# Performance work log

Measured on AMD Instinct MI355X. Metric: run time of the kernel, lower is better.

Reference implementation:

```python
import jax, jax.numpy as jnp
import numpy as np


def setup_inputs() -> dict:
    key = jax.random.key(0)
    k1, k2 = jax.random.split(key)
    N, D, K = 262144, 64, 1024
    residual = jax.random.normal(k1, (N, D), dtype=jnp.float32)
    # nn.init.uniform_(codebook.weight, -1/K, 1/K)
    codebook = jax.random.uniform(k2, (K, D), dtype=jnp.float32,
                                  minval=-1.0 / K, maxval=1.0 / K)
    return {"residual": residual, "codebook": codebook}


def reference(residual, codebook):
    # squared L2 distances via ||a||^2 + ||b||^2 - 2 a.b (argmin-equivalent to
    # the broadcast (N,K,D) form, without materializing it)
    r2 = jnp.sum(residual * residual, axis=1, keepdims=True)        # (N, 1)
    c2 = jnp.sum(codebook * codebook, axis=1)[None, :]              # (1, K)
    dists = r2 + c2 - 2.0 * (residual @ codebook.T)                 # (N, K)
    codes = jnp.argmin(dists, axis=1)                               # (N,) int
    quantized = codebook[codes]                                     # (N, D)
    return quantized, codes
```

## Files before the change

kernel.cpp:

```cpp
#include <hip/hip_runtime.h>
#include <float.h>

#define D 64

typedef float f32x4 __attribute__((ext_vector_type(4)));
typedef _Float16 f16x8 __attribute__((ext_vector_type(8)));

__device__ __forceinline__ float np_sum_sq_64(const float* v) {
  float s[8];
#pragma unroll
  for (int j = 0; j < 8; ++j) s[j] = __fmul_rn(v[j], v[j]);
#pragma unroll
  for (int b = 1; b < 8; ++b) {
#pragma unroll
    for (int j = 0; j < 8; ++j)
      s[j] = __fadd_rn(s[j], __fmul_rn(v[8 * b + j], v[8 * b + j]));
  }
  float t01 = __fadd_rn(s[0], s[1]);
  float t23 = __fadd_rn(s[2], s[3]);
  float t45 = __fadd_rn(s[4], s[5]);
  float t67 = __fadd_rn(s[6], s[7]);
  return __fadd_rn(__fadd_rn(t01, t23), __fadd_rn(t45, t67));
}

__device__ __forceinline__ unsigned int pkh(float a, float b) {
  union { _Float16 h[2]; unsigned int u; } x;
  x.h[0] = (_Float16)a;
  x.h[1] = (_Float16)b;
  return x.u;
}

__global__ __launch_bounds__(64) void vq_prep(
    const float* __restrict__ cb, unsigned short* __restrict__ cbh,
    float4* __restrict__ cbT4, float* __restrict__ c2,
    float* __restrict__ c2n, unsigned int* __restrict__ counters, int K) {
  if (blockIdx.x == 0 && threadIdx.x == 0) { counters[0] = 0u; counters[1] = 0u; }
  int k = blockIdx.x * 64 + threadIdx.x;
  if (k >= K) return;
  float row[D];
  const float4* cp = (const float4*)(cb + (size_t)k * D);
#pragma unroll
  for (int i = 0; i < 16; ++i) {
    float4 v = cp[i];
    row[4 * i] = v.x; row[4 * i + 1] = v.y;
    row[4 * i + 2] = v.z; row[4 * i + 3] = v.w;
    cbT4[(size_t)i * K + k] = v;
    *(uint2*)(cbh + (size_t)k * D + 4 * i) =
        make_uint2(pkh(v.x * 1024.f, v.y * 1024.f),
                   pkh(v.z * 1024.f, v.w * 1024.f));
  }
  float c2v = np_sum_sq_64(row);
  c2[k] = c2v;
  c2n[k] = -512.0f * c2v;
}

__global__ __launch_bounds__(256, 3) void vq_screen(
    const float* __restrict__ residual, const float* __restrict__ codebook,
    const unsigned short* __restrict__ cbh, const float* __restrict__ c2n,
    float* __restrict__ out_q, float* __restrict__ codes_f,
    unsigned int* __restrict__ counters, int* __restrict__ list,
    int N, int K) {
  __shared__ unsigned short smem[4096];
  __shared__ float red[768];
  __shared__ int code_lds[64];
  __shared__ float srow[64];

  int tid = threadIdx.x;
  int rowbase = blockIdx.x * 64;

  float sr4[4];
#pragma unroll
  for (int jj = 0; jj < 4; ++jj) {
    int i = tid + 256 * jj;
    int r = i >> 4, d0 = (i & 15) * 4;
    float4 v = *(const float4*)(residual + (size_t)(rowbase + r) * D + d0);
    sr4[jj] = fabsf(v.x) + fabsf(v.y) + fabsf(v.z) + fabsf(v.w);
    int tile = r >> 4, rr = r & 15;
    int kblk = d0 >> 5, kk = d0 & 31;
    int lanep = rr + 16 * (kk >> 3);
    int off = ((tile * 2 + kblk) * 64 + lanep) * 8 + (kk & 7);
    *(uint2*)(smem + off) = make_uint2(pkh(v.x, v.y), pkh(v.z, v.w));
  }
#pragma unroll
  for (int jj = 0; jj < 4; ++jj) {
    float s = sr4[jj];
    s += __shfl_xor(s, 1, 64);
    s += __shfl_xor(s, 2, 64);
    s += __shfl_xor(s, 4, 64);
    s += __shfl_xor(s, 8, 64);
    sr4[jj] = s;
  }
  if ((tid & 15) == 0) {
#pragma unroll
    for (int jj = 0; jj < 4; ++jj) srow[(tid >> 4) + 16 * jj] = sr4[jj];
  }
  __syncthreads();

  int w = tid >> 6, lane = tid & 63;
  int lane15 = lane & 15, lq = lane >> 4;

  f16x8 ah[4][2];
#pragma unroll
  for (int t = 0; t < 4; ++t)
#pragma unroll
    for (int kb = 0; kb < 2; ++kb)
      ah[t][kb] = *(const f16x8*)(smem + ((t * 2 + kb) * 64 + lane) * 8);

  float m1[4][4], m2[4][4], m3[4][4];
#pragma unroll
  for (int t = 0; t < 4; ++t)
#pragma unroll
    for (int j = 0; j < 4; ++j) {
      m1[t][j] = -FLT_MAX; m2[t][j] = -FLT_MAX; m3[t][j] = -FLT_MAX;
    }

  const unsigned short* ph = cbh + (size_t)(w * 16 + lane15) * D + lq * 8;
  const float* pc2 = c2n + (w * 16 + lane15);

  f16x8 B0a = *(const f16x8*)(ph);
  f16x8 B1a = *(const f16x8*)(ph + 32);
  float c2a = *pc2;
  ph += 64 * D; pc2 += 64;
  f16x8 B0b = *(const f16x8*)(ph);
  f16x8 B1b = *(const f16x8*)(ph + 32);
  float c2b = *pc2;

  unsigned int idb = (unsigned int)((w << 4) | lane15);
  for (int cc = 0; cc < 16; ++cc) {
    f16x8 ch0 = B0a, ch1 = B1a;
    float q = c2a;
    B0a = B0b; B1a = B1b; c2a = c2b;
    if (cc < 14) {
      ph += 64 * D; pc2 += 64;
      B0b = *(const f16x8*)(ph);
      B1b = *(const f16x8*)(ph + 32);
      c2b = *pc2;
    }

#pragma unroll
    for (int t = 0; t < 4; ++t) {
      f32x4 a = {q, q, q, q};
      a = __builtin_amdgcn_mfma_f32_16x16x32_f16(ah[t][0], ch0, a, 0, 0, 0);
      a = __builtin_amdgcn_mfma_f32_16x16x32_f16(ah[t][1], ch1, a, 0, 0, 0);
#pragma unroll
      for (int j = 0; j < 4; ++j) {
        float spf = __uint_as_float((__float_as_uint(a[j]) & 0xFFFFFC00u) | idb);
        float o1 = m1[t][j], o2 = m2[t][j];
        m3[t][j] = __builtin_amdgcn_fmed3f(o2, m3[t][j], spf);
        m2[t][j] = __builtin_amdgcn_fmed3f(o1, o2, spf);
        m1[t][j] = fmaxf(o1, spf);
      }
    }
    idb += 64u;
  }

#pragma unroll
  for (int dlt = 1; dlt < 16; dlt <<= 1) {
#pragma unroll
    for (int t = 0; t < 4; ++t)
#pragma unroll
      for (int j = 0; j < 4; ++j) {
        float a1 = m1[t][j], a2 = m2[t][j], a3 = m3[t][j];
        float b1 = __shfl_xor(a1, dlt, 64);
        float b2 = __shfl_xor(a2, dlt, 64);
        float b3 = __shfl_xor(a3, dlt, 64);
        m1[t][j] = fmaxf(a1, b1);
        m2[t][j] = fmaxf(fminf(a1, b1), fmaxf(a2, b2));
        m3[t][j] = fmaxf(fmaxf(fminf(a2, b1), fminf(a1, b2)), fmaxf(a3, b3));
      }
  }

  if (lane15 == 0) {
#pragma unroll
    for (int t = 0; t < 4; ++t)
#pragma unroll
      for (int j = 0; j < 4; ++j) {
        int r = t * 16 + lq * 4 + j;
        int base = (w * 64 + r) * 3;
        red[base + 0] = m1[t][j];
        red[base + 1] = m2[t][j];
        red[base + 2] = m3[t][j];
      }
  }
  __syncthreads();
  if (tid < 64) {
    float a1 = red[tid * 3 + 0], a2 = red[tid * 3 + 1], a3 = red[tid * 3 + 2];
#pragma unroll
    for (int wv = 1; wv < 4; ++wv) {
      float b1 = red[(wv * 64 + tid) * 3 + 0];
      float b2 = red[(wv * 64 + tid) * 3 + 1];
      float b3 = red[(wv * 64 + tid) * 3 + 2];
      float n1 = fmaxf(a1, b1);
      float n2 = fmaxf(fminf(a1, b1), fmaxf(a2, b2));
      float n3 = fmaxf(fmaxf(fminf(a2, b1), fminf(a1, b2)), fmaxf(a3, b3));
      a1 = n1; a2 = n2; a3 = n3;
    }
    unsigned int u1 = __float_as_uint(a1);
    unsigned int u2 = __float_as_uint(a2);
    unsigned int u3 = __float_as_uint(a3);
    int ka = (int)(u1 & 1023u);
    float g1 = __uint_as_float(u1 & 0xFFFFFC00u);
    float g2 = __uint_as_float(u2 & 0xFFFFFC00u);
    float g3 = __uint_as_float(u3 & 0xFFFFFC00u);
    float margin = __builtin_fmaf(srow[tid], 2.3552e-3f, 2.048e-2f);
    int row = rowbase + tid;
    code_lds[tid] = ka;
    float cf = (float)ka;
    if (g1 - g2 < margin) {
      if (g1 - g3 < margin) {
        unsigned int s = atomicAdd(counters + 0, 1u);
        list[s] = row;
      } else {
        unsigned int s = atomicAdd(counters + 1, 1u);
        list[N - 1 - (int)s] = row;
        cf = (float)(int)((unsigned int)ka | ((u2 & 1023u) << 10));
      }
    }
    codes_f[row] = cf;
  }
  __syncthreads();

  for (int e = tid; e < 4096; e += 256) {
    int r = e >> 6, d = e & 63;
    out_q[(size_t)rowbase * D + e] = codebook[((size_t)code_lds[r] << 6) + d];
  }
}

__global__ __launch_bounds__(256) void vq_pair(
    const float* __restrict__ residual, const float* __restrict__ codebook,
    const float* __restrict__ c2, float* __restrict__ codes_f,
    float* __restrict__ out_q, const unsigned int* __restrict__ counters,
    const int* __restrict__ list, int N) {
  unsigned int cnt = counters[1];
  for (unsigned int i = blockIdx.x * 256 + threadIdx.x; i < cnt;
       i += gridDim.x * 256) {
    int row = list[N - 1 - (int)i];
    int packed = (int)codes_f[row];
    int ka = packed & 1023, kb = packed >> 10;

    float r[D];
    const float4* rp = (const float4*)(residual + ((size_t)row << 6));
#pragma unroll
    for (int q = 0; q < 16; ++q) {
      float4 v = rp[q];
      r[4 * q] = v.x; r[4 * q + 1] = v.y; r[4 * q + 2] = v.z; r[4 * q + 3] = v.w;
    }
    float r2 = np_sum_sq_64(r);

    float da = 0.f, db = 0.f;
    const float4* ap = (const float4*)(codebook + ((size_t)ka << 6));
    const float4* bp = (const float4*)(codebook + ((size_t)kb << 6));
#pragma unroll
    for (int q = 0; q < 16; ++q) {
      float4 x = ap[q], y = bp[q];
      da = __fmaf_rn(r[4 * q + 0], x.x, da); db = __fmaf_rn(r[4 * q + 0], y.x, db);
      da = __fmaf_rn(r[4 * q + 1], x.y, da); db = __fmaf_rn(r[4 * q + 1], y.y, db);
      da = __fmaf_rn(r[4 * q + 2], x.z, da); db = __fmaf_rn(r[4 * q + 2], y.z, db);
      da = __fmaf_rn(r[4 * q + 3], x.w, da); db = __fmaf_rn(r[4 * q + 3], y.w, db);
    }
    float dista = __fsub_rn(__fadd_rn(r2, c2[ka]), __fmul_rn(2.0f, da));
    float distb = __fsub_rn(__fadd_rn(r2, c2[kb]), __fmul_rn(2.0f, db));
    bool bwin = (distb < dista) || (distb == dista && kb < ka);
    int win = bwin ? kb : ka;
    codes_f[row] = (float)win;
    if (bwin) {
      float4* oq = (float4*)(out_q + ((size_t)row << 6));
      const float4* cw = (const float4*)(codebook + ((size_t)win << 6));
#pragma unroll
      for (int q = 0; q < 16; ++q) oq[q] = cw[q];
    }
  }
}

__global__ __launch_bounds__(256) void vq_rescore(
    const float* __restrict__ residual, const float* __restrict__ codebook,
    const float4* __restrict__ cbT4, const float* __restrict__ c2,
    float* __restrict__ codes_f, float* __restrict__ out_q,
    const unsigned int* __restrict__ counters,
    const int* __restrict__ list, int K) {
  unsigned int cnt = counters[0];
  int w = threadIdx.x >> 6, lane = threadIdx.x & 63;
  unsigned int npairs = (cnt + 1) >> 1;
  for (unsigned int g = blockIdx.x * 4 + w; g < npairs; g += gridDim.x * 4) {
    int n0 = list[2 * g];
    bool two = (2 * g + 1 < cnt);
    int n1 = two ? list[2 * g + 1] : n0;

    float rl0 = residual[(size_t)n0 * D + lane];
    float rl1 = residual[(size_t)n1 * D + lane];

    int j = lane & 7;
    float x0 = __shfl(rl0, j, 64), x1 = __shfl(rl1, j, 64);
    float s0 = __fmul_rn(x0, x0), s1 = __fmul_rn(x1, x1);
#pragma unroll
    for (int b = 1; b < 8; ++b) {
      x0 = __shfl(rl0, 8 * b + j, 64);
      x1 = __shfl(rl1, 8 * b + j, 64);
      s0 = __fadd_rn(s0, __fmul_rn(x0, x0));
      s1 = __fadd_rn(s1, __fmul_rn(x1, x1));
    }
    s0 = __fadd_rn(s0, __shfl_xor(s0, 1, 64));
    s1 = __fadd_rn(s1, __shfl_xor(s1, 1, 64));
    s0 = __fadd_rn(s0, __shfl_xor(s0, 2, 64));
    s1 = __fadd_rn(s1, __shfl_xor(s1, 2, 64));
    s0 = __fadd_rn(s0, __shfl_xor(s0, 4, 64));
    s1 = __fadd_rn(s1, __shfl_xor(s1, 4, 64));
    float r2_0 = s0, r2_1 = s1;

    float m0[16], m1v[16];
#pragma unroll
    for (int ch = 0; ch < 16; ++ch) { m0[ch] = 0.f; m1v[ch] = 0.f; }

    for (int d4 = 0; d4 < 16; ++d4) {
      float a0 = __shfl(rl0, 4 * d4, 64), b0 = __shfl(rl0, 4 * d4 + 1, 64);
      float c0 = __shfl(rl0, 4 * d4 + 2, 64), e0 = __shfl(rl0, 4 * d4 + 3, 64);
      float a1 = __shfl(rl1, 4 * d4, 64), b1 = __shfl(rl1, 4 * d4 + 1, 64);
      float c1 = __shfl(rl1, 4 * d4 + 2, 64), e1 = __shfl(rl1, 4 * d4 + 3, 64);
      const float4* bp = cbT4 + (size_t)d4 * K + lane;
      float4 cbv[8];
#pragma unroll
      for (int h = 0; h < 2; ++h) {
#pragma unroll
        for (int q = 0; q < 8; ++q) cbv[q] = bp[(h * 8 + q) * 64];
#pragma unroll
        for (int q = 0; q < 8; ++q) {
          int ch = h * 8 + q;
          float4 c = cbv[q];
          float t0 = m0[ch], t1 = m1v[ch];
          t0 = __fmaf_rn(a0, c.x, t0); t1 = __fmaf_rn(a1, c.x, t1);
          t0 = __fmaf_rn(b0, c.y, t0); t1 = __fmaf_rn(b1, c.y, t1);
          t0 = __fmaf_rn(c0, c.z, t0); t1 = __fmaf_rn(c1, c.z, t1);
          t0 = __fmaf_rn(e0, c.w, t0); t1 = __fmaf_rn(e1, c.w, t1);
          m0[ch] = t0; m1v[ch] = t1;
        }
      }
    }

    float best0 = FLT_MAX, best1 = FLT_MAX;
    int bk0 = 0, bk1 = 0;
#pragma unroll
    for (int ch = 0; ch < 16; ++ch) {
      int code = ch * 64 + lane;
      float c2v = c2[code];
      float d0 = __fsub_rn(__fadd_rn(r2_0, c2v), __fmul_rn(2.0f, m0[ch]));
      float d1 = __fsub_rn(__fadd_rn(r2_1, c2v), __fmul_rn(2.0f, m1v[ch]));
      if (d0 < best0) { best0 = d0; bk0 = code; }
      if (d1 < best1) { best1 = d1; bk1 = code; }
    }
#pragma unroll
    for (int off = 32; off > 0; off >>= 1) {
      float ob = __shfl_down(best0, off, 64);
      int oi = __shfl_down(bk0, off, 64);
      if (ob < best0 || (ob == best0 && oi < bk0)) { best0 = ob; bk0 = oi; }
      ob = __shfl_down(best1, off, 64);
      oi = __shfl_down(bk1, off, 64);
      if (ob < best1 || (ob == best1 && oi < bk1)) { best1 = ob; bk1 = oi; }
    }
    int k0 = __shfl(bk0, 0, 64);
    int k1 = __shfl(bk1, 0, 64);
    if (lane == 0) codes_f[n0] = (float)k0;
    out_q[(size_t)n0 * D + lane] = codebook[((size_t)k0 << 6) + lane];
    if (two) {
      if (lane == 0) codes_f[n1] = (float)k1;
      out_q[(size_t)n1 * D + lane] = codebook[((size_t)k1 << 6) + lane];
    }
  }
}

extern "C" void kernel_launch(void* const* d_in, const int* in_sizes, int n_in,
                              void* d_out, int out_size, void* d_ws, size_t ws_size,
                              hipStream_t stream) {
  const float* residual = (const float*)d_in[0];
  const float* codebook = (const float*)d_in[1];
  int N = in_sizes[0] / D;
  int K = in_sizes[1] / D;

  float* out_q = (float*)d_out;
  float* codes_f = out_q + (size_t)N * D;

  char* ws = (char*)d_ws;
  float* c2 = (float*)ws;
  float* c2n = (float*)(ws + (size_t)K * 4);
  unsigned short* cbh = (unsigned short*)(ws + (size_t)K * 8);
  float4* cbT4 = (float4*)(ws + (size_t)K * 8 + (size_t)K * D * 2);
  unsigned int* counters =
      (unsigned int*)(ws + (size_t)K * 8 + (size_t)K * D * 2 + (size_t)K * D * 4);
  int* list = (int*)(counters + 2);

  vq_prep<<<(K + 63) / 64, 64, 0, stream>>>(codebook, cbh, cbT4, c2, c2n,
                                            counters, K);

  vq_screen<<<N / 64, 256, 0, stream>>>(residual, codebook, cbh, c2n, out_q,
                                        codes_f, counters, list, N, K);

  vq_pair<<<512, 256, 0, stream>>>(residual, codebook, c2, codes_f, out_q,
                                   counters, list, N);

  vq_rescore<<<2048, 256, 0, stream>>>(residual, codebook, cbT4, c2, codes_f,
                                       out_q, counters, list, K);
}
```

Baseline: 246.6 us.

## Fuse two-candidate pair rescoring into screen kernel and shrink rescore grid

Rows whose top two fp16 scores are close but the third is clear are now resolved inside vq_screen with an exact fp32 distance comparison. Previously they were appended to a list and handled by a separate vq_pair kernel. This removes one kernel launch, an atomic and list write per such row, and the later re-gather and out_q rewrite. In exchange, some threads run a divergent 64-wide fp32 dot-product path inside the screen kernel, which adds register pressure under launch_bounds(256,3). The rescore grid also drops from 2048 to 512 blocks.

```diff
diff --git a/kernel.cpp b/kernel.cpp
--- a/kernel.cpp
+++ b/kernel.cpp
@@ -57,9 +57,9 @@
 __global__ __launch_bounds__(256, 3) void vq_screen(
     const float* __restrict__ residual, const float* __restrict__ codebook,
     const unsigned short* __restrict__ cbh, const float* __restrict__ c2n,
-    float* __restrict__ out_q, float* __restrict__ codes_f,
-    unsigned int* __restrict__ counters, int* __restrict__ list,
-    int N, int K) {
+    const float* __restrict__ c2, float* __restrict__ out_q,
+    float* __restrict__ codes_f, unsigned int* __restrict__ counters,
+    int* __restrict__ list, int N, int K) {
   __shared__ unsigned short smem[4096];
   __shared__ float red[768];
   __shared__ int code_lds[64];
@@ -204,71 +204,47 @@
     float g3 = __uint_as_float(u3 & 0xFFFFFC00u);
     float margin = __builtin_fmaf(srow[tid], 2.3552e-3f, 2.048e-2f);
     int row = rowbase + tid;
-    code_lds[tid] = ka;
-    float cf = (float)ka;
+    int win = ka;
     if (g1 - g2 < margin) {
       if (g1 - g3 < margin) {
         unsigned int s = atomicAdd(counters + 0, 1u);
         list[s] = row;
       } else {
-        unsigned int s = atomicAdd(counters + 1, 1u);
-        list[N - 1 - (int)s] = row;
-        cf = (float)(int)((unsigned int)ka | ((u2 & 1023u) << 10));
-      }
-    }
-    codes_f[row] = cf;
+        int kb = (int)(u2 & 1023u);
+        float r[D];
+        const float4* rp = (const float4*)(residual + ((size_t)row << 6));
+#pragma unroll
+        for (int qq = 0; qq < 16; ++qq) {
+          float4 v = rp[qq];
+          r[4 * qq] = v.x; r[4 * qq + 1] = v.y;
+          r[4 * qq + 2] = v.z; r[4 * qq + 3] = v.w;
+        }
+        float r2 = np_sum_sq_64(r);
+        float da = 0.f, db = 0.f;
+        const float4* ap = (const float4*)(codebook + ((size_t)ka << 6));
+        const float4* bp = (const float4*)(codebook + ((size_t)kb << 6));
+#pragma unroll
+        for (int qq = 0; qq < 16; ++qq) {
+          float4 x = ap[qq], y = bp[qq];
+          da = __fmaf_rn(r[4 * qq + 0], x.x, da); db = __fmaf_rn(r[4 * qq + 0], y.x, db);
+          da = __fmaf_rn(r[4 * qq + 1], x.y, da); db = __fmaf_rn(r[4 * qq + 1], y.y, db);
+          da = __fmaf_rn(r[4 * qq + 2], x.z, da); db = __fmaf_rn(r[4 * qq + 2], y.z, db);
+          da = __fmaf_rn(r[4 * qq + 3], x.w, da); db = __fmaf_rn(r[4 * qq + 3], y.w, db);
+        }
+        float dista = __fsub_rn(__fadd_rn(r2, c2[ka]), __fmul_rn(2.0f, da));
+        float distb = __fsub_rn(__fadd_rn(r2, c2[kb]), __fmul_rn(2.0f, db));
+        bool bwin = (distb < dista) || (distb == dista && kb < ka);
+        win = bwin ? kb : ka;
+      }
+    }
+    code_lds[tid] = win;
+    codes_f[row] = (float)win;
   }
   __syncthreads();
 
   for (int e = tid; e < 4096; e += 256) {
     int r = e >> 6, d = e & 63;
     out_q[(size_t)rowbase * D + e] = codebook[((size_t)code_lds[r] << 6) + d];
-  }
-}
-
-__global__ __launch_bounds__(256) void vq_pair(
-    const float* __restrict__ residual, const float* __restrict__ codebook,
-    const float* __restrict__ c2, float* __restrict__ codes_f,
-    float* __restrict__ out_q, const unsigned int* __restrict__ counters,
-    const int* __restrict__ list, int N) {
-  unsigned int cnt = counters[1];
-  for (unsigned int i = blockIdx.x * 256 + threadIdx.x; i < cnt;
-       i += gridDim.x * 256) {
-    int row = list[N - 1 - (int)i];
-    int packed = (int)codes_f[row];
-    int ka = packed & 1023, kb = packed >> 10;
-
-    float r[D];
-    const float4* rp = (const float4*)(residual + ((size_t)row << 6));
-#pragma unroll
-    for (int q = 0; q < 16; ++q) {
-      float4 v = rp[q];
-      r[4 * q] = v.x; r[4 * q + 1] = v.y; r[4 * q + 2] = v.z; r[4 * q + 3] = v.w;
-    }
-    float r2 = np_sum_sq_64(r);
-
-    float da = 0.f, db = 0.f;
-    const float4* ap = (const float4*)(codebook + ((size_t)ka << 6));
-    const float4* bp = (const float4*)(codebook + ((size_t)kb << 6));
-#pragma unroll
-    for (int q = 0; q < 16; ++q) {
-      float4 x = ap[q], y = bp[q];
-      da = __fmaf_rn(r[4 * q + 0], x.x, da); db = __fmaf_rn(r[4 * q + 0], y.x, db);
-      da = __fmaf_rn(r[4 * q + 1], x.y, da); db = __fmaf_rn(r[4 * q + 1], y.y, db);
-      da = __fmaf_rn(r[4 * q + 2], x.z, da); db = __fmaf_rn(r[4 * q + 2], y.z, db);
-      da = __fmaf_rn(r[4 * q + 3], x.w, da); db = __fmaf_rn(r[4 * q + 3], y.w, db);
-    }
-    float dista = __fsub_rn(__fadd_rn(r2, c2[ka]), __fmul_rn(2.0f, da));
-    float distb = __fsub_rn(__fadd_rn(r2, c2[kb]), __fmul_rn(2.0f, db));
-    bool bwin = (distb < dista) || (distb == dista && kb < ka);
-    int win = bwin ? kb : ka;
-    codes_f[row] = (float)win;
-    if (bwin) {
-      float4* oq = (float4*)(out_q + ((size_t)row << 6));
-      const float4* cw = (const float4*)(codebook + ((size_t)win << 6));
-#pragma unroll
-      for (int q = 0; q < 16; ++q) oq[q] = cw[q];
-    }
   }
 }
 
@@ -390,12 +366,9 @@
   vq_prep<<<(K + 63) / 64, 64, 0, stream>>>(codebook, cbh, cbT4, c2, c2n,
                                             counters, K);
 
-  vq_screen<<<N / 64, 256, 0, stream>>>(residual, codebook, cbh, c2n, out_q,
-                                        codes_f, counters, list, N, K);
-
-  vq_pair<<<512, 256, 0, stream>>>(residual, codebook, c2, codes_f, out_q,
-                                   counters, list, N);
-
-  vq_rescore<<<2048, 256, 0, stream>>>(residual, codebook, cbT4, c2, codes_f,
-                                       out_q, counters, list, K);
-}
+  vq_screen<<<N / 64, 256, 0, stream>>>(residual, codebook, cbh, c2n, c2,
+                                        out_q, codes_f, counters, list, N, K);
+
+  vq_rescore<<<512, 256, 0, stream>>>(residual, codebook, cbT4, c2, codes_f,
+                                      out_q, counters, list, K);
+}
```

Measured after the change: 225.4 us. 1.09x faster.
